# Kernel tuning notes

Hardware: AMD Instinct MI355X
Metric: run time of the kernel (lower is better)

The kernel has to match this reference:

```python
import jax, jax.numpy as jnp
import numpy as np
from jax import lax

B, S, H, T = 64, 512, 1024, 24


def setup_inputs() -> dict:
    key = jax.random.key(0)
    k1, k2, k3, k4, k5 = jax.random.split(key, 5)
    feats = jax.random.normal(k1, (B, S, H), dtype=jnp.float32)
    target = jax.random.randint(k2, (B, S), 0, T)  # tag ids (argmax of original one-hot target)
    # descending-sorted lengths -> prefix mask, matching the torch code's sorted-batch assumption
    lengths = jnp.sort(jax.random.randint(k3, (B,), S // 2, S + 1))[::-1]
    mask = jnp.arange(S)[None, :] < lengths[:, None]  # (B,S) bool
    # hidden2tag params (uniform init ~ nn.Linear default scale)
    bound = 1.0 / np.sqrt(H)
    W = jax.random.uniform(k4, (T, H), minval=-bound, maxval=bound, dtype=jnp.float32)
    b = jax.random.uniform(k5, (T,), minval=-bound, maxval=bound, dtype=jnp.float32)
    transition = jnp.zeros((T, T), dtype=jnp.float32)
    return {"feats": feats, "target": target, "mask": mask, "W": W, "b": b, "transition": transition}


def reference(feats, target, mask, W, b, transition):
    # emission scores: (B,S,T)
    emission = jnp.einsum("bsh,th->bst", feats, W) + b
    # gold path score
    sc = jnp.take_along_axis(emission, target[:, :, None], axis=2).squeeze(-1)  # (B,S)
    sc = sc.at[:, 1:].add(transition[target[:, :-1], target[:, 1:]])
    total_score = (sc * mask.astype(emission.dtype)).sum(axis=1)  # (B,)
    # forward algorithm (log-partition) as a scan over time
    p0 = emission[:, 0]  # (B,T)
    emis_t = jnp.swapaxes(emission[:, 1:], 0, 1)  # (S-1,B,T)
    mask_t = jnp.swapaxes(mask[:, 1:], 0, 1)      # (S-1,B)

    def step(p, xs):
        emit_i, m_i = xs
        # log_sum[b, prev, cur] = p[b, prev] + transition[prev, cur] + emit_i[b, cur]
        new_p = jax.nn.logsumexp(p[:, :, None] + transition[None, :, :] + emit_i[:, None, :], axis=1)
        return jnp.where(m_i[:, None], new_p, p), None

    p, _ = lax.scan(step, p0, (emis_t, mask_t))
    log_Z = jax.nn.logsumexp(p, axis=1)  # (B,)
    loss = -jnp.mean(total_score - log_Z)
    return loss, emission
```

## Files before the change

### kernel.cpp

```cpp
#include <hip/hip_runtime.h>
#include <cstdint>
#include <math.h>

#define B_ 64
#define S_ 512
#define H_ 1024
#define T_ 24
#define TP_ 32

typedef unsigned int u32;
typedef unsigned short u16;
typedef __attribute__((ext_vector_type(8))) short short8v;
typedef __attribute__((ext_vector_type(4))) float f32x4;
typedef __attribute__((ext_vector_type(4))) u32 uint4v;

__device__ __forceinline__ float rl_f32(float x, int sl) {
    return __uint_as_float(__builtin_amdgcn_readlane(__float_as_uint(x), sl));
}

__device__ __forceinline__ void split_pk(float f0, float f1, u32& hpk, u32& lpk) {
    const u32 u0 = __float_as_uint(f0), u1 = __float_as_uint(f1);
    const u32 t1 = u1 & 0xffff0000u;
    hpk = (u0 >> 16) | t1;
    const float fl0 = f0 - __uint_as_float(u0 & 0xffff0000u);
    const float fl1 = f1 - __uint_as_float(t1);
    lpk = (__float_as_uint(fl0) >> 16) | (__float_as_uint(fl1) & 0xffff0000u);
}

__global__ __launch_bounds__(256) void wcvt_kernel(const float* __restrict__ W,
                                                   u16* __restrict__ Wh,
                                                   u16* __restrict__ Wl,
                                                   float* __restrict__ out) {
    const int i = blockIdx.x * 256 + threadIdx.x;
    if (i == 0) out[0] = 0.f;
    const int t = i >> 10;
    const float f = (t < T_) ? W[i] : 0.f;
    const u32 u = __float_as_uint(f);
    const u32 rh = u + 0x7fffu + ((u >> 16) & 1u);
    const u16 hb = (u16)(rh >> 16);
    const float fh = __uint_as_float((u32)hb << 16);
    const float fl = f - fh;
    const u32 u2 = __float_as_uint(fl);
    const u32 rl2 = u2 + 0x7fffu + ((u2 >> 16) & 1u);
    Wh[i] = hb;
    Wl[i] = (u16)(rl2 >> 16);
}

__global__ __launch_bounds__(256) void gemm_kernel(const float* __restrict__ feats,
                                                   const u16* __restrict__ Wh,
                                                   const u16* __restrict__ Wl,
                                                   const float* __restrict__ bias,
                                                   float* __restrict__ emission) {
    const int tid  = threadIdx.x;
    const int lane = tid & 63;
    const int wv   = tid >> 6;
    const int r16  = lane & 15;
    const int g    = lane >> 4;
    const int mtile = blockIdx.x * 4 + wv;

    const float* ap  = feats + ((long)mtile * 16 + r16) * H_ + g * 8;
    const u16* bh0p = Wh + r16 * H_ + g * 8;
    const u16* bl0p = Wl + r16 * H_ + g * 8;
    const u16* bh1p = Wh + (r16 + 16) * H_ + g * 8;
    const u16* bl1p = Wl + (r16 + 16) * H_ + g * 8;

    f32x4 acc0 = {0.f, 0.f, 0.f, 0.f};
    f32x4 acc1 = {0.f, 0.f, 0.f, 0.f};

#pragma unroll 4
    for (int kk = 0; kk < H_ / 32; ++kk) {
        const int ko = kk * 32;
        const float4 a0 = *(const float4*)(ap + ko);
        const float4 a1 = *(const float4*)(ap + ko + 4);
        const short8v bh0 = *(const short8v*)(bh0p + ko);
        const short8v bl0 = *(const short8v*)(bl0p + ko);
        const short8v bh1 = *(const short8v*)(bh1p + ko);
        const short8v bl1 = *(const short8v*)(bl1p + ko);

        u32 h0, l0, h1, l1, h2, l2, h3, l3;
        split_pk(a0.x, a0.y, h0, l0);
        split_pk(a0.z, a0.w, h1, l1);
        split_pk(a1.x, a1.y, h2, l2);
        split_pk(a1.z, a1.w, h3, l3);
        const uint4v hv = {h0, h1, h2, h3};
        const uint4v lv = {l0, l1, l2, l3};
        const short8v ah = __builtin_bit_cast(short8v, hv);
        const short8v al = __builtin_bit_cast(short8v, lv);

        acc0 = __builtin_amdgcn_mfma_f32_16x16x32_bf16(al, bh0, acc0, 0, 0, 0);
        acc0 = __builtin_amdgcn_mfma_f32_16x16x32_bf16(ah, bl0, acc0, 0, 0, 0);
        acc0 = __builtin_amdgcn_mfma_f32_16x16x32_bf16(ah, bh0, acc0, 0, 0, 0);
        acc1 = __builtin_amdgcn_mfma_f32_16x16x32_bf16(al, bh1, acc1, 0, 0, 0);
        acc1 = __builtin_amdgcn_mfma_f32_16x16x32_bf16(ah, bl1, acc1, 0, 0, 0);
        acc1 = __builtin_amdgcn_mfma_f32_16x16x32_bf16(ah, bh1, acc1, 0, 0, 0);
    }

    const float b0 = bias[r16];
    const float b1 = (r16 + 16 < T_) ? bias[r16 + 16] : 0.f;
    float* op = emission + ((long)mtile * 16 + g * 4) * T_;
#pragma unroll
    for (int r = 0; r < 4; ++r) {
        op[r * T_ + r16] = acc0[r] + b0;
        if (r16 + 16 < T_) op[r * T_ + r16 + 16] = acc1[r] + b1;
    }
}

#define DECL_E(i) const float E##i = __expf(trans[(i) * T_ + jj]);
#define FMA4(i0, i1, i2, i3)                                                   \
    s0 = fmaf(rl_f32(q, i0), E##i0, s0);                                       \
    s1 = fmaf(rl_f32(q, i1), E##i1, s1);                                       \
    s2 = fmaf(rl_f32(q, i2), E##i2, s2);                                       \
    s3 = fmaf(rl_f32(q, i3), E##i3, s3);

__global__ __launch_bounds__(64, 1) void scan_kernel(const float* __restrict__ emission,
                                                     const int* __restrict__ target,
                                                     const int* __restrict__ mask,
                                                     const float* __restrict__ trans,
                                                     float* __restrict__ out) {
    const int b = blockIdx.x;
    const int j = threadIdx.x;
    const int jj = j < 24 ? j : 23;

    const float* em = emission + (long)b * S_ * T_;
    const int* mk = mask + b * S_;

    int mc = 0;
#pragma unroll
    for (int k = 0; k < 8; ++k) mc += mk[j + k * 64];
#pragma unroll
    for (int off = 32; off; off >>= 1) mc += __shfl_xor(mc, off);
    const int len = __builtin_amdgcn_readfirstlane(mc);

    DECL_E(0)  DECL_E(1)  DECL_E(2)  DECL_E(3)  DECL_E(4)  DECL_E(5)
    DECL_E(6)  DECL_E(7)  DECL_E(8)  DECL_E(9)  DECL_E(10) DECL_E(11)
    DECL_E(12) DECL_E(13) DECL_E(14) DECL_E(15) DECL_E(16) DECL_E(17)
    DECL_E(18) DECL_E(19) DECL_E(20) DECL_E(21) DECL_E(22) DECL_E(23)

    float q = (j < 24) ? __expf(em[j]) : 0.f;
    float C = 0.f;

    float lb[8];
#pragma unroll
    for (int k = 0; k < 8; ++k) lb[k] = em[(1 + k) * T_ + jj];

    for (int sb = 1; sb < S_; sb += 16) {
#pragma unroll
        for (int k = 0; k < 16; ++k) {
            const int s = sb + k;
            const float X = __expf(lb[k & 7]);
            const int sp = s + 8;
            lb[k & 7] = (sp < S_) ? em[sp * T_ + jj] : 0.f;

            if (s < len) {
                float s0 = 0.f, s1 = 0.f, s2 = 0.f, s3 = 0.f;
                FMA4(0, 1, 2, 3)
                FMA4(4, 5, 6, 7)
                FMA4(8, 9, 10, 11)
                FMA4(12, 13, 14, 15)
                FMA4(16, 17, 18, 19)
                FMA4(20, 21, 22, 23)
                q = ((s0 + s1) + (s2 + s3)) * X;
            }
        }
        const float r = rl_f32(q, 0);
        q *= (1.0f / r);
        C += __logf(r);
    }

    float ex = (j < 24) ? q : 0.f;
#pragma unroll
    for (int off = 32; off; off >>= 1) ex += __shfl_down(ex, off);

    float ssum = 0.f;
#pragma unroll
    for (int kk = 0; kk < S_ / 64; ++kk) {
        const int s = j + kk * 64;
        if (mk[s]) {
            const int tg = target[b * S_ + s];
            float v = em[s * T_ + tg];
            if (s > 0) v += trans[target[b * S_ + s - 1] * T_ + tg];
            ssum += v;
        }
    }
#pragma unroll
    for (int off = 32; off; off >>= 1) ssum += __shfl_down(ssum, off);

    if (j == 0) {
        const float logZ = C + __logf(ex);
        atomicAdd(out, (logZ - ssum) * (1.0f / B_));
    }
}

extern "C" void kernel_launch(void* const* d_in, const int* in_sizes, int n_in,
                              void* d_out, int out_size, void* d_ws, size_t ws_size,
                              hipStream_t stream) {
    const float* feats  = (const float*)d_in[0];
    const int*   target = (const int*)d_in[1];
    const int*   mask   = (const int*)d_in[2];
    const float* W      = (const float*)d_in[3];
    const float* bias   = (const float*)d_in[4];
    const float* trans  = (const float*)d_in[5];

    float* out = (float*)d_out;
    float* emission = out + 1;
    u16* Wh = (u16*)d_ws;
    u16* Wl = Wh + TP_ * H_;

    wcvt_kernel<<<(TP_ * H_) / 256, 256, 0, stream>>>(W, Wh, Wl, out);
    gemm_kernel<<<512, 256, 0, stream>>>(feats, Wh, Wl, bias, emission);
    scan_kernel<<<64, 64, 0, stream>>>(emission, target, mask, trans, out);
}
```

Before: 285.0 us.

## Parallelize CRF forward scan by chunked transfer-matrix products across time

New measurement: 290.7 us. No clear change (+2.0%).

```diff
diff --git a/kernel.cpp b/kernel.cpp
--- a/kernel.cpp
+++ b/kernel.cpp
@@ -7,6 +7,9 @@
 #define H_ 1024
 #define T_ 24
 #define TP_ 32
+#define NC_ 8
+#define CL_ 64
+#define CSTRIDE_ 600
 
 typedef unsigned int u32;
 typedef unsigned short u16;
@@ -106,18 +109,31 @@
 }
 
 #define DECL_E(i) const float E##i = __expf(trans[(i) * T_ + jj]);
-#define FMA4(i0, i1, i2, i3)                                                   \
-    s0 = fmaf(rl_f32(q, i0), E##i0, s0);                                       \
-    s1 = fmaf(rl_f32(q, i1), E##i1, s1);                                       \
-    s2 = fmaf(rl_f32(q, i2), E##i2, s2);                                       \
-    s3 = fmaf(rl_f32(q, i3), E##i3, s3);
-
-__global__ __launch_bounds__(64, 1) void scan_kernel(const float* __restrict__ emission,
-                                                     const int* __restrict__ target,
-                                                     const int* __restrict__ mask,
-                                                     const float* __restrict__ trans,
-                                                     float* __restrict__ out) {
-    const int b = blockIdx.x;
+#define FMA4M(mv, i0, i1, i2, i3)                                              \
+    s0 = fmaf(rl_f32(mv, i0), E##i0, s0);                                      \
+    s1 = fmaf(rl_f32(mv, i1), E##i1, s1);                                      \
+    s2 = fmaf(rl_f32(mv, i2), E##i2, s2);                                      \
+    s3 = fmaf(rl_f32(mv, i3), E##i3, s3);
+#define UPDATE(mv)                                                             \
+    {                                                                          \
+        float s0 = 0.f, s1 = 0.f, s2 = 0.f, s3 = 0.f;                          \
+        FMA4M(mv, 0, 1, 2, 3)                                                  \
+        FMA4M(mv, 4, 5, 6, 7)                                                  \
+        FMA4M(mv, 8, 9, 10, 11)                                                \
+        FMA4M(mv, 12, 13, 14, 15)                                              \
+        FMA4M(mv, 16, 17, 18, 19)                                              \
+        FMA4M(mv, 20, 21, 22, 23)                                              \
+        mv = ((s0 + s1) + (s2 + s3)) * X;                                      \
+    }
+
+__global__ __launch_bounds__(64, 1) void chunk_kernel(const float* __restrict__ emission,
+                                                      const int* __restrict__ mask,
+                                                      const float* __restrict__ trans,
+                                                      float* __restrict__ wsM) {
+    const int bid = blockIdx.x;
+    const int w = bid & 7;
+    const int c = (bid >> 3) & (NC_ - 1);
+    const int b = bid >> 6;
     const int j = threadIdx.x;
     const int jj = j < 24 ? j : 23;
 
@@ -136,38 +152,94 @@
     DECL_E(12) DECL_E(13) DECL_E(14) DECL_E(15) DECL_E(16) DECL_E(17)
     DECL_E(18) DECL_E(19) DECL_E(20) DECL_E(21) DECL_E(22) DECL_E(23)
 
-    float q = (j < 24) ? __expf(em[j]) : 0.f;
-    float C = 0.f;
+    const int lo = 1 + c * CL_;
+    const int hi = min(lo + CL_, S_);
+    const int send = min(hi, len);
+    const int r0 = 3 * w;
+
+    float m0 = (jj == r0 + 0) ? 1.f : 0.f;
+    float m1 = (jj == r0 + 1) ? 1.f : 0.f;
+    float m2 = (jj == r0 + 2) ? 1.f : 0.f;
+    float Cw = 0.f;
 
     float lb[8];
 #pragma unroll
-    for (int k = 0; k < 8; ++k) lb[k] = em[(1 + k) * T_ + jj];
-
-    for (int sb = 1; sb < S_; sb += 16) {
-#pragma unroll
-        for (int k = 0; k < 16; ++k) {
+    for (int k = 0; k < 8; ++k) lb[k] = em[(lo + k) * T_ + jj];
+
+    for (int sb = lo; sb < hi; sb += 8) {
+#pragma unroll
+        for (int k = 0; k < 8; ++k) {
             const int s = sb + k;
-            const float X = __expf(lb[k & 7]);
+            const float X = __expf(lb[k]);
             const int sp = s + 8;
-            lb[k & 7] = (sp < S_) ? em[sp * T_ + jj] : 0.f;
-
-            if (s < len) {
-                float s0 = 0.f, s1 = 0.f, s2 = 0.f, s3 = 0.f;
-                FMA4(0, 1, 2, 3)
-                FMA4(4, 5, 6, 7)
-                FMA4(8, 9, 10, 11)
-                FMA4(12, 13, 14, 15)
-                FMA4(16, 17, 18, 19)
-                FMA4(20, 21, 22, 23)
-                q = ((s0 + s1) + (s2 + s3)) * X;
+            lb[k] = (sp < S_) ? em[sp * T_ + jj] : 0.f;
+            if (s < send) {
+                UPDATE(m0)
+                UPDATE(m1)
+                UPDATE(m2)
             }
         }
-        const float r = rl_f32(q, 0);
-        q *= (1.0f / r);
+        float r = m0;
+#pragma unroll
+        for (int off = 32; off; off >>= 1) r = fmaxf(r, __shfl_xor(r, off));
+        const float inv = 1.0f / r;
+        m0 *= inv;
+        m1 *= inv;
+        m2 *= inv;
+        Cw += __logf(r);
+    }
+
+    float* outp = wsM + (long)(b * NC_ + c) * CSTRIDE_;
+    if (j < 24) {
+        outp[(r0 + 0) * 24 + j] = m0;
+        outp[(r0 + 1) * 24 + j] = m1;
+        outp[(r0 + 2) * 24 + j] = m2;
+    }
+    if (j == 0) {
+        outp[576 + r0 + 0] = Cw;
+        outp[576 + r0 + 1] = Cw;
+        outp[576 + r0 + 2] = Cw;
+    }
+}
+
+__global__ __launch_bounds__(64) void finalize_kernel(const float* __restrict__ emission,
+                                                      const int* __restrict__ target,
+                                                      const int* __restrict__ mask,
+                                                      const float* __restrict__ trans,
+                                                      const float* __restrict__ wsM,
+                                                      float* __restrict__ out) {
+    const int b = blockIdx.x;
+    const int j = threadIdx.x;
+    const int jj = j < 24 ? j : 23;
+    const float* em = emission + (long)b * S_ * T_;
+    const int* mk = mask + b * S_;
+
+    float p = (j < 24) ? __expf(em[j]) : 0.f;
+    float C = 0.f;
+
+    for (int c = 0; c < NC_; ++c) {
+        const float* Mc = wsM + (long)(b * NC_ + c) * CSTRIDE_;
+        float Ls = (j < 24) ? Mc[576 + j] : -3.0e38f;
+        float Lmax = Ls;
+#pragma unroll
+        for (int off = 32; off; off >>= 1) Lmax = fmaxf(Lmax, __shfl_xor(Lmax, off));
+        p *= __expf(Ls - Lmax);
+        C += Lmax;
+        float s0 = 0.f, s1 = 0.f, s2 = 0.f, s3 = 0.f;
+#pragma unroll
+        for (int t = 0; t < 24; t += 4) {
+            s0 = fmaf(rl_f32(p, t + 0), Mc[(t + 0) * 24 + jj], s0);
+            s1 = fmaf(rl_f32(p, t + 1), Mc[(t + 1) * 24 + jj], s1);
+            s2 = fmaf(rl_f32(p, t + 2), Mc[(t + 2) * 24 + jj], s2);
+            s3 = fmaf(rl_f32(p, t + 3), Mc[(t + 3) * 24 + jj], s3);
+        }
+        p = (j < 24) ? ((s0 + s1) + (s2 + s3)) : 0.f;
+        const float r = rl_f32(p, 0);
+        p *= (1.0f / r);
         C += __logf(r);
     }
 
-    float ex = (j < 24) ? q : 0.f;
+    float ex = p;
 #pragma unroll
     for (int off = 32; off; off >>= 1) ex += __shfl_down(ex, off);
 
@@ -205,8 +277,10 @@
     float* emission = out + 1;
     u16* Wh = (u16*)d_ws;
     u16* Wl = Wh + TP_ * H_;
+    float* wsM = (float*)((char*)d_ws + 131072);
 
     wcvt_kernel<<<(TP_ * H_) / 256, 256, 0, stream>>>(W, Wh, Wl, out);
     gemm_kernel<<<512, 256, 0, stream>>>(feats, Wh, Wl, bias, emission);
-    scan_kernel<<<64, 64, 0, stream>>>(emission, target, mask, trans, out);
-}
+    chunk_kernel<<<B_ * NC_ * 8, 64, 0, stream>>>(emission, mask, trans, wsM);
+    finalize_kernel<<<B_, 64, 0, stream>>>(emission, target, mask, trans, wsM, out);
+}
```

## Parallelize CRF forward scan via chunked transfer-matrix products on MFMA

Applied to the files above, without the earlier changes.

Result: faster. 260.0 us (-8.8%).

```diff
diff --git a/kernel.cpp b/kernel.cpp
--- a/kernel.cpp
+++ b/kernel.cpp
@@ -7,6 +7,9 @@
 #define H_ 1024
 #define T_ 24
 #define TP_ 32
+#define NC_ 32
+#define CL_ 16
+#define KST_ 1040
 
 typedef unsigned int u32;
 typedef unsigned short u16;
@@ -105,69 +108,215 @@
     }
 }
 
-#define DECL_E(i) const float E##i = __expf(trans[(i) * T_ + jj]);
-#define FMA4(i0, i1, i2, i3)                                                   \
-    s0 = fmaf(rl_f32(q, i0), E##i0, s0);                                       \
-    s1 = fmaf(rl_f32(q, i1), E##i1, s1);                                       \
-    s2 = fmaf(rl_f32(q, i2), E##i2, s2);                                       \
-    s3 = fmaf(rl_f32(q, i3), E##i3, s3);
-
-__global__ __launch_bounds__(64, 1) void scan_kernel(const float* __restrict__ emission,
-                                                     const int* __restrict__ target,
-                                                     const int* __restrict__ mask,
-                                                     const float* __restrict__ trans,
-                                                     float* __restrict__ out) {
+__global__ __launch_bounds__(64, 1) void chunk_kernel(const float* __restrict__ emission,
+                                                      const int* __restrict__ mask,
+                                                      const float* __restrict__ trans,
+                                                      float* __restrict__ wsK) {
+    __shared__ u32 lds[2][2][16][18];
+    const int bid = blockIdx.x;
+    const int c_ = bid & (NC_ - 1);
+    const int b  = bid >> 5;
+    const int l  = threadIdx.x;
+    const int cc = l & 15;
+    const int q  = l >> 4;
+    const int aq4 = (l & 48);
+
+    const float* em = emission + (long)b * S_ * T_;
+    const int* mk = mask + b * S_;
+
+    int mc = 0;
+#pragma unroll
+    for (int k = 0; k < 8; ++k) mc += mk[l + k * 64];
+#pragma unroll
+    for (int off = 32; off; off >>= 1) mc += __shfl_xor(mc, off);
+    const int len = __builtin_amdgcn_readfirstlane(mc);
+
+    const int lo = 1 + c_ * CL_;
+    const int hi = min(lo + CL_, S_);
+    const int send = min(hi, len);
+
+    short8v Ah[2], Al[2];
+#pragma unroll
+    for (int I = 0; I < 2; ++I) {
+        const int j = 16 * I + cc;
+        u32 hw[4], lw[4];
+#pragma unroll
+        for (int w = 0; w < 4; ++w) {
+            const int t0 = 8 * q + 2 * w;
+            const float v0 = (t0 < 24 && j < 24) ? __expf(trans[t0 * T_ + j]) : 0.f;
+            const float v1 = (t0 + 1 < 24 && j < 24) ? __expf(trans[(t0 + 1) * T_ + j]) : 0.f;
+            split_pk(v0, v1, hw[w], lw[w]);
+        }
+        const uint4v hv = {hw[0], hw[1], hw[2], hw[3]};
+        const uint4v lv = {lw[0], lw[1], lw[2], lw[3]};
+        Ah[I] = __builtin_bit_cast(short8v, hv);
+        Al[I] = __builtin_bit_cast(short8v, lv);
+    }
+
+    f32x4 K[2][2];
+#pragma unroll
+    for (int I = 0; I < 2; ++I)
+#pragma unroll
+        for (int J = 0; J < 2; ++J)
+#pragma unroll
+            for (int r = 0; r < 4; ++r)
+                K[I][J][r] = (16 * I + 4 * q + r == 16 * J + cc) ? 1.f : 0.f;
+
+    u32 bh[2][4], bl[2][4];
+#pragma unroll
+    for (int J = 0; J < 2; ++J)
+#pragma unroll
+        for (int w = 0; w < 4; ++w) {
+            const int k0 = 8 * q + 2 * w, col = 16 * J + cc;
+            bh[J][w] = (k0 == col ? 0x3f80u : 0u) | (k0 + 1 == col ? 0x3f800000u : 0u);
+            bl[J][w] = 0u;
+        }
+
+    const int xj = ((l & 31) < 24) ? (l & 31) : 0;
+    float xr_[CL_];
+#pragma unroll
+    for (int k = 0; k < CL_; ++k) {
+        const int s = lo + k;
+        xr_[k] = em[((s < S_) ? s : 0) * T_ + xj];
+    }
+
+    float Ls = 0.f;
+    const f32x4 z4 = {0.f, 0.f, 0.f, 0.f};
+
+#pragma unroll
+    for (int k = 0; k < CL_; ++k) {
+        const int s = lo + k;
+        if (s < send) {
+            const uint4v bh0v = {bh[0][0], bh[0][1], bh[0][2], bh[0][3]};
+            const uint4v bh1v = {bh[1][0], bh[1][1], bh[1][2], bh[1][3]};
+            const uint4v bl0v = {bl[0][0], bl[0][1], bl[0][2], bl[0][3]};
+            const uint4v bl1v = {bl[1][0], bl[1][1], bl[1][2], bl[1][3]};
+            const short8v B0h = __builtin_bit_cast(short8v, bh0v);
+            const short8v B1h = __builtin_bit_cast(short8v, bh1v);
+            const short8v B0l = __builtin_bit_cast(short8v, bl0v);
+            const short8v B1l = __builtin_bit_cast(short8v, bl1v);
+
+            f32x4 acc[2][2];
+#pragma unroll
+            for (int I = 0; I < 2; ++I) {
+                acc[I][0] = __builtin_amdgcn_mfma_f32_16x16x32_bf16(Ah[I], B0h, z4, 0, 0, 0);
+                acc[I][0] = __builtin_amdgcn_mfma_f32_16x16x32_bf16(Ah[I], B0l, acc[I][0], 0, 0, 0);
+                acc[I][0] = __builtin_amdgcn_mfma_f32_16x16x32_bf16(Al[I], B0h, acc[I][0], 0, 0, 0);
+                acc[I][1] = __builtin_amdgcn_mfma_f32_16x16x32_bf16(Ah[I], B1h, z4, 0, 0, 0);
+                acc[I][1] = __builtin_amdgcn_mfma_f32_16x16x32_bf16(Ah[I], B1l, acc[I][1], 0, 0, 0);
+                acc[I][1] = __builtin_amdgcn_mfma_f32_16x16x32_bf16(Al[I], B1h, acc[I][1], 0, 0, 0);
+            }
+
+            const float X = __expf(xr_[k]);
+            const int xi = __float_as_int(X);
+            float xr0[4], xr1[4];
+#pragma unroll
+            for (int r = 0; r < 4; ++r) {
+                xr0[r] = __int_as_float(__builtin_amdgcn_ds_bpermute(aq4 + 4 * r, xi));
+                xr1[r] = __int_as_float(__builtin_amdgcn_ds_bpermute(aq4 + 64 + 4 * r, xi));
+            }
+#pragma unroll
+            for (int J = 0; J < 2; ++J)
+#pragma unroll
+                for (int r = 0; r < 4; ++r) {
+                    K[0][J][r] = acc[0][J][r] * xr0[r];
+                    K[1][J][r] = acc[1][J][r] * xr1[r];
+                }
+
+            if (k == 7 || k == CL_ - 1) {
+                float mx = K[0][0][0];
+#pragma unroll
+                for (int I = 0; I < 2; ++I)
+#pragma unroll
+                    for (int J = 0; J < 2; ++J)
+#pragma unroll
+                        for (int r = 0; r < 4; ++r) mx = fmaxf(mx, K[I][J][r]);
+#pragma unroll
+                for (int off = 32; off; off >>= 1) mx = fmaxf(mx, __shfl_xor(mx, off));
+                const u32 ef = __float_as_uint(mx) & 0x7f800000u;
+                const float inv = __uint_as_float(0x7f000000u - ef);
+#pragma unroll
+                for (int I = 0; I < 2; ++I)
+#pragma unroll
+                    for (int J = 0; J < 2; ++J)
+#pragma unroll
+                        for (int r = 0; r < 4; ++r) K[I][J][r] *= inv;
+                Ls += (float)((int)(ef >> 23) - 127) * 0.6931471805599453f;
+            }
+
+            if (k < CL_ - 1) {
+#pragma unroll
+                for (int I = 0; I < 2; ++I)
+#pragma unroll
+                    for (int J = 0; J < 2; ++J)
+#pragma unroll
+                        for (int m = 0; m < 2; ++m) {
+                            u32 h, lo_w;
+                            split_pk(K[I][J][2 * m], K[I][J][2 * m + 1], h, lo_w);
+                            const int p = 8 * I + 2 * q + m;
+                            lds[0][J][p][cc] = h;
+                            lds[1][J][p][cc] = lo_w;
+                        }
+#pragma unroll
+                for (int J = 0; J < 2; ++J)
+#pragma unroll
+                    for (int w = 0; w < 4; ++w) {
+                        bh[J][w] = lds[0][J][4 * q + w][cc];
+                        bl[J][w] = lds[1][J][4 * q + w][cc];
+                    }
+            }
+        }
+    }
+
+    float* outp = wsK + (long)(b * NC_ + c_) * KST_;
+#pragma unroll
+    for (int I = 0; I < 2; ++I)
+#pragma unroll
+        for (int J = 0; J < 2; ++J)
+#pragma unroll
+            for (int r = 0; r < 4; ++r)
+                outp[(16 * I + 4 * q + r) * 32 + 16 * J + cc] = K[I][J][r];
+    if (l == 0) outp[1024] = Ls;
+}
+
+#define ACC4(kv, t0)                                                           \
+    s0 = fmaf(rl_f32(p, (t0) + 0), kv.x, s0);                                  \
+    s1 = fmaf(rl_f32(p, (t0) + 1), kv.y, s1);                                  \
+    s2 = fmaf(rl_f32(p, (t0) + 2), kv.z, s2);                                  \
+    s3 = fmaf(rl_f32(p, (t0) + 3), kv.w, s3);
+
+__global__ __launch_bounds__(64) void finalize_kernel(const float* __restrict__ emission,
+                                                      const int* __restrict__ target,
+                                                      const int* __restrict__ mask,
+                                                      const float* __restrict__ trans,
+                                                      const float* __restrict__ wsK,
+                                                      float* __restrict__ out) {
     const int b = blockIdx.x;
     const int j = threadIdx.x;
     const int jj = j < 24 ? j : 23;
-
     const float* em = emission + (long)b * S_ * T_;
     const int* mk = mask + b * S_;
 
-    int mc = 0;
-#pragma unroll
-    for (int k = 0; k < 8; ++k) mc += mk[j + k * 64];
-#pragma unroll
-    for (int off = 32; off; off >>= 1) mc += __shfl_xor(mc, off);
-    const int len = __builtin_amdgcn_readfirstlane(mc);
-
-    DECL_E(0)  DECL_E(1)  DECL_E(2)  DECL_E(3)  DECL_E(4)  DECL_E(5)
-    DECL_E(6)  DECL_E(7)  DECL_E(8)  DECL_E(9)  DECL_E(10) DECL_E(11)
-    DECL_E(12) DECL_E(13) DECL_E(14) DECL_E(15) DECL_E(16) DECL_E(17)
-    DECL_E(18) DECL_E(19) DECL_E(20) DECL_E(21) DECL_E(22) DECL_E(23)
-
-    float q = (j < 24) ? __expf(em[j]) : 0.f;
+    float p = (j < 24) ? __expf(em[j]) : 0.f;
     float C = 0.f;
 
-    float lb[8];
-#pragma unroll
-    for (int k = 0; k < 8; ++k) lb[k] = em[(1 + k) * T_ + jj];
-
-    for (int sb = 1; sb < S_; sb += 16) {
-#pragma unroll
-        for (int k = 0; k < 16; ++k) {
-            const int s = sb + k;
-            const float X = __expf(lb[k & 7]);
-            const int sp = s + 8;
-            lb[k & 7] = (sp < S_) ? em[sp * T_ + jj] : 0.f;
-
-            if (s < len) {
-                float s0 = 0.f, s1 = 0.f, s2 = 0.f, s3 = 0.f;
-                FMA4(0, 1, 2, 3)
-                FMA4(4, 5, 6, 7)
-                FMA4(8, 9, 10, 11)
-                FMA4(12, 13, 14, 15)
-                FMA4(16, 17, 18, 19)
-                FMA4(20, 21, 22, 23)
-                q = ((s0 + s1) + (s2 + s3)) * X;
-            }
-        }
-        const float r = rl_f32(q, 0);
-        q *= (1.0f / r);
-        C += __logf(r);
-    }
-
-    float ex = (j < 24) ? q : 0.f;
+    for (int c = 0; c < NC_; ++c) {
+        const float* base = wsK + (long)(b * NC_ + c) * KST_;
+        C += base[1024];
+        const float4* rp = (const float4*)(base + jj * 32);
+        const float4 k0 = rp[0], k1 = rp[1], k2 = rp[2], k3 = rp[3], k4 = rp[4], k5 = rp[5];
+        float s0 = 0.f, s1 = 0.f, s2 = 0.f, s3 = 0.f;
+        ACC4(k0, 0) ACC4(k1, 4) ACC4(k2, 8) ACC4(k3, 12) ACC4(k4, 16) ACC4(k5, 20)
+        p = (j < 24) ? ((s0 + s1) + (s2 + s3)) : 0.f;
+        float mx = p;
+#pragma unroll
+        for (int off = 32; off; off >>= 1) mx = fmaxf(mx, __shfl_xor(mx, off));
+        const u32 ef = __float_as_uint(mx) & 0x7f800000u;
+        p *= __uint_as_float(0x7f000000u - ef);
+        C += (float)((int)(ef >> 23) - 127) * 0.6931471805599453f;
+    }
+
+    float ex = p;
 #pragma unroll
     for (int off = 32; off; off >>= 1) ex += __shfl_down(ex, off);
 
@@ -205,8 +354,10 @@
     float* emission = out + 1;
     u16* Wh = (u16*)d_ws;
     u16* Wl = Wh + TP_ * H_;
+    float* wsK = (float*)((char*)d_ws + 131072);
 
     wcvt_kernel<<<(TP_ * H_) / 256, 256, 0, stream>>>(W, Wh, Wl, out);
     gemm_kernel<<<512, 256, 0, stream>>>(feats, Wh, Wl, bias, emission);
-    scan_kernel<<<64, 64, 0, stream>>>(emission, target, mask, trans, out);
-}
+    chunk_kernel<<<B_ * NC_, 64, 0, stream>>>(emission, mask, trans, wsK);
+    finalize_kernel<<<B_, 64, 0, stream>>>(emission, target, mask, trans, wsK, out);
+}
```
